# Optimization experiments

Hardware: AMD Instinct MI355X
Metric: run time of the kernel (lower is better)

## Reference

```python
import jax, jax.numpy as jnp
import numpy as np

H, P, HID, CHUNK = 8, 128, 1024, 256  # num_heads, head_dim, hidden_size, chunk_size
EPS = 1e-5


def segsum(x):
    """x: [..., L] -> [..., L, L] with out[t, s] = sum_{s+1..t} x, -inf above diagonal."""
    L = x.shape[-1]
    cs = jnp.cumsum(x, axis=-1)
    s = cs[..., :, None] - cs[..., None, :]
    mask = jnp.tril(jnp.ones((L, L), dtype=bool))
    return jnp.where(mask, s, -jnp.inf)


def ssd(X, dA, Bm, Cm, chunk):
    """Chunked Mamba2 scan (ssd_minimal_discrete).
    X:  [b, t, h, p]  (already discretized: dt * x)
    dA: [b, t, h]     (dt * A, per-head scalar decays)
    Bm, Cm: [b, t, h, n]
    """
    b, t, h, p = X.shape
    c = t // chunk
    X = X.reshape(b, c, chunk, h, p)
    Bm = Bm.reshape(b, c, chunk, h, -1)
    Cm = Cm.reshape(b, c, chunk, h, -1)
    dA = dA.reshape(b, c, chunk, h).transpose(0, 3, 1, 2)  # [b, h, c, l]
    Acs = jnp.cumsum(dA, axis=-1)                          # [b, h, c, l]
    Lm = jnp.exp(segsum(dA))                               # [b, h, c, l, l]
    # intra-chunk (diagonal blocks)
    Y_diag = jnp.einsum('bclhn,bcshn,bhcls,bcshp->bclhp', Cm, Bm, Lm, X)
    # per-chunk state contribution
    decay_states = jnp.exp(Acs[..., -1:] - Acs)            # [b, h, c, l]
    states = jnp.einsum('bclhn,bhcl,bclhp->bchpn', Bm, decay_states, X)
    # inter-chunk recurrence (vectorized via segsum over chunk decays)
    A_last = Acs[..., -1]                                  # [b, h, c]
    decay_chunk = jnp.exp(segsum(jnp.pad(A_last, ((0, 0), (0, 0), (1, 0)))))  # [b,h,c+1,c+1]
    states = jnp.concatenate([jnp.zeros_like(states[:, :1]), states], axis=1)  # [b, c+1, h, p, n]
    new_states = jnp.einsum('bhzc,bchpn->bzhpn', decay_chunk, states)
    prev = new_states[:, :-1]                              # states entering each chunk
    out_decay = jnp.exp(Acs)                               # [b, h, c, l]
    Y_off = jnp.einsum('bclhn,bchpn,bhcl->bclhp', Cm, prev, out_decay)
    return (Y_diag + Y_off).reshape(b, t, h, p)


def setup_inputs() -> dict:
    key = jax.random.key(0)
    ks = jax.random.split(key, 6)
    B, T = 2, 4096
    hidden_states = jax.random.normal(ks[0], (B, T, HID), dtype=jnp.float32)
    dt_W = 0.01 * jax.random.normal(ks[1], (H, HID), dtype=jnp.float32)
    dt_b = jnp.zeros((H,), jnp.float32)
    g_W = 0.02 * jax.random.normal(ks[2], (H, HID), dtype=jnp.float32)
    g_b = jnp.zeros((H,), jnp.float32)
    A_log = jnp.log(jnp.arange(1, H + 1, dtype=jnp.float32))
    D = jnp.ones((H,), jnp.float32)
    dt_bias = jnp.ones((H,), jnp.float32)
    norm_weight = jnp.ones((H * P,), jnp.float32)
    o_W = jax.random.normal(ks[3], (H, P, P), dtype=jnp.float32) / np.sqrt(P)
    o_b = jnp.zeros((H, P), jnp.float32)
    return dict(hidden_states=hidden_states, dt_W=dt_W, dt_b=dt_b, g_W=g_W, g_b=g_b,
                A_log=A_log, D=D, dt_bias=dt_bias, norm_weight=norm_weight, o_W=o_W, o_b=o_b)


def reference(hidden_states, dt_W, dt_b, g_W, g_b, A_log, D, dt_bias, norm_weight, o_W, o_b):
    B, T, _ = hidden_states.shape
    dt = hidden_states @ dt_W.T + dt_b                 # [B, T, H]
    gate = jnp.tanh(hidden_states @ g_W.T + g_b)       # [B, T, H]
    gate_full = jnp.repeat(gate, P, axis=-1)           # repeat_interleave -> [B, T, H*P]
    A = -jnp.exp(A_log)                                # [H]
    x = hidden_states.reshape(B, T, H, P)
    dt_eff = dt + dt_bias                              # dt_bias applied inside the kernel
    Y = ssd(x * dt_eff[..., None], dt_eff * A, x, x, CHUNK)  # B = C = x per source
    Y = Y + D[None, None, :, None] * x                 # skip term
    # RMSNormGated, norm_before_gate=False: norm(y * silu(gate))
    z = Y.reshape(B, T, H * P) * jax.nn.silu(gate_full)
    z = z * jax.lax.rsqrt(jnp.mean(z * z, axis=-1, keepdims=True) + EPS) * norm_weight
    last = z.reshape(B, T, H, P)[:, -1]                # out[:, -1, :, :]
    o = jnp.einsum('bhp,hpq->bhq', last, o_W) + o_b    # GroupLinear (per-head)
    return o.reshape(B, H * P)
```

## Files before the change

### kernel.cpp

```cpp
#include <hip/hip_runtime.h>
#include <math.h>

#define NH 8
#define NP 128
#define HID 1024
#define TT 4096
#define BB 2
#define WIN 256
#define NDT (BB * WIN / 4)

#define WS_XD 4096
#define WS_SG 8192
#define WS_ZQ 8208
#define WS_U  8224
#define WS_CTRL 10272

__global__ __launch_bounds__(256) void k_pre(const float* __restrict__ hid,
                                             const float* __restrict__ dtW,
                                             const float* __restrict__ dtb,
                                             const float* __restrict__ dtbias,
                                             const float* __restrict__ gW,
                                             const float* __restrict__ gb,
                                             float* __restrict__ dtEff,
                                             float* __restrict__ xdot,
                                             float* __restrict__ sgate_g,
                                             int* __restrict__ ctrl) {
    __shared__ float sW[NH * HID];
    __shared__ float sXL[HID];
    int tid = threadIdx.x;
    int idx = blockIdx.x;
    if (idx == 0 && tid == 0) ctrl[0] = 0;
    bool isGate = (idx >= NDT);
    int b = isGate ? (idx - NDT) : (idx >> 6);

    const float* Wsrc = isGate ? gW : dtW;
    for (int i = tid * 4; i < NH * HID; i += 1024)
        *(float4*)&sW[i] = *(const float4*)&Wsrc[i];
    const float* xl = hid + ((size_t)b * TT + TT - 1) * HID;
    *(float4*)&sXL[tid * 4] = *(const float4*)&xl[tid * 4];
    __syncthreads();

    int wave = tid >> 6, lane = tid & 63;
    int twin = isGate ? (WIN - 1) : ((idx & 63) * 4 + wave);
    const float* hrow = hid + ((size_t)b * TT + (TT - WIN) + twin) * HID;

    float acc[NH];
#pragma unroll
    for (int h = 0; h < NH; ++h) acc[h] = 0.f;
    float pd[4];

#pragma unroll
    for (int i = 0; i < 4; ++i) {
        float4 v = *(const float4*)&hrow[i * 256 + lane * 4];
#pragma unroll
        for (int h = 0; h < NH; ++h) {
            float4 w = *(const float4*)&sW[h * HID + i * 256 + lane * 4];
            acc[h] += v.x * w.x + v.y * w.y + v.z * w.z + v.w * w.w;
        }
        float4 x4 = *(const float4*)&sXL[i * 256 + lane * 4];
        pd[i] = v.x * x4.x + v.y * x4.y + v.z * x4.z + v.w * x4.w;
    }

#pragma unroll
    for (int h = 0; h < NH; ++h) {
        float a = acc[h];
#pragma unroll
        for (int off = 32; off >= 1; off >>= 1) a += __shfl_xor(a, off, 64);
        acc[h] = a;
    }

    if (isGate) {
        if (tid == 0) {
#pragma unroll
            for (int h = 0; h < NH; ++h) {
                float g = tanhf(acc[h] + gb[h]);
                sgate_g[b * NH + h] = g / (1.f + expf(-g));
            }
        }
        return;
    }

#pragma unroll
    for (int i = 0; i < 4; ++i) {
#pragma unroll
        for (int off = 16; off >= 1; off >>= 1) pd[i] += __shfl_xor(pd[i], off, 32);
    }

    if (lane == 0) {
#pragma unroll
        for (int h = 0; h < NH; ++h)
            dtEff[(b * NH + h) * WIN + twin] = acc[h] + dtb[h] + dtbias[h];
#pragma unroll
        for (int i = 0; i < 4; ++i)
            xdot[(b * NH + 2 * i) * WIN + twin] = pd[i];
    }
    if (lane == 32) {
#pragma unroll
        for (int i = 0; i < 4; ++i)
            xdot[(b * NH + 2 * i + 1) * WIN + twin] = pd[i];
    }
}

__global__ __launch_bounds__(256) void k_fin(const float* __restrict__ hid,
                                             const float* __restrict__ dtEff,
                                             const float* __restrict__ xdot,
                                             const float* __restrict__ A_log,
                                             const float* __restrict__ Dv,
                                             const float* __restrict__ sgate_g,
                                             const float* __restrict__ normw,
                                             const float* __restrict__ oW,
                                             const float* __restrict__ ob,
                                             float* __restrict__ u_g,
                                             float* __restrict__ zsq_g,
                                             int* __restrict__ ctrl,
                                             float* __restrict__ out) {
    int bh = blockIdx.x;
    int b = bh >> 3, h = bh & 7;
    int tid = threadIdx.x, wave = tid >> 6, lane = tid & 63;

    __shared__ float sWT[4];
    __shared__ float scoef[WIN];
    __shared__ int sMinR;
    __shared__ float sacc[2][NP];
    __shared__ float sred[2];
    __shared__ float szn[NP];
    __shared__ float4 sa4[8][32];
    __shared__ int sLast;

    if (tid == 0) sMinR = WIN - 1;

    float A = -expf(A_log[h]);
    float mydt = dtEff[bh * WIN + tid];
    float myxd = xdot[bh * WIN + tid];
    float dA = mydt * A;

    float x = dA;
#pragma unroll
    for (int off = 1; off < 64; off <<= 1) {
        float v = __shfl_down(x, off, 64);
        if (lane + off < 64) x += v;
    }
    if (lane == 0) sWT[wave] = x;
    __syncthreads();
    float offs = 0.f;
    for (int w = wave + 1; w < 4; ++w) offs += sWT[w];
    float e = x + offs - dA;

    float coef = 0.f;
    if (e > -104.f) {
        coef = expf(e) * mydt * myxd;
        atomicMin(&sMinR, tid);
    }
    scoef[tid] = coef;
    __syncthreads();

    int r0 = sMinR;
    int tt = tid >> 7, pp = tid & 127;
    const float* xb = hid + ((size_t)b * TT + (TT - WIN)) * HID + h * NP;
    float acc = 0.f;
    for (int r = r0 + tt; r < WIN; r += 2)
        acc += scoef[r] * xb[(size_t)r * HID + pp];
    sacc[tt][pp] = acc;
    __syncthreads();

    if (tid < NP) {
        float xlv = hid[((size_t)b * TT + TT - 1) * HID + h * NP + tid];
        float z = (sacc[0][tid] + sacc[1][tid] + Dv[h] * xlv) * sgate_g[bh];
        szn[tid] = z * normw[h * NP + tid];
        float s = z * z;
#pragma unroll
        for (int off = 32; off >= 1; off >>= 1) s += __shfl_xor(s, off, 64);
        if ((tid & 63) == 0) sred[tid >> 6] = s;
    }
    __syncthreads();
    if (tid == 0) zsq_g[bh] = sred[0] + sred[1];

    int qg = tid & 31, seg = tid >> 5;
    const float* Wb = oW + (size_t)h * NP * NP;
    float4 a = {0.f, 0.f, 0.f, 0.f};
#pragma unroll
    for (int j = 0; j < 16; ++j) {
        int p = seg * 16 + j;
        float zv = szn[p];
        float4 w = *(const float4*)&Wb[p * NP + 4 * qg];
        a.x += zv * w.x; a.y += zv * w.y; a.z += zv * w.z; a.w += zv * w.w;
    }
    sa4[seg][qg] = a;
    __syncthreads();

    if (tid < 32) {
        float4 r = sa4[0][tid];
#pragma unroll
        for (int s = 1; s < 8; ++s) {
            float4 v = sa4[s][tid];
            r.x += v.x; r.y += v.y; r.z += v.z; r.w += v.w;
        }
        *(float4*)&u_g[bh * NP + 4 * tid] = r;
    }

    __syncthreads();
    if (tid == 0) {
        __threadfence();
        int t = __hip_atomic_fetch_add(&ctrl[0], 1, __ATOMIC_ACQ_REL,
                                       __HIP_MEMORY_SCOPE_AGENT);
        sLast = (t == BB * NH - 1) ? 1 : 0;
    }
    __syncthreads();
    if (!sLast) return;
    if (tid == 0) __threadfence();
    __syncthreads();

    float s0 = 0.f, s1 = 0.f;
#pragma unroll
    for (int i = 0; i < NH; ++i) {
        s0 += zsq_g[i];
        s1 += zsq_g[NH + i];
    }
    float sc0 = rsqrtf(s0 / (float)HID + 1e-5f);
    float sc1 = rsqrtf(s1 / (float)HID + 1e-5f);

#pragma unroll
    for (int k = 0; k < 8; ++k) {
        int c = tid + k * 256;
        float sc = (c >> 10) ? sc1 : sc0;
        out[c] = u_g[c] * sc + ob[c & 1023];
    }
}

extern "C" void kernel_launch(void* const* d_in, const int* in_sizes, int n_in,
                              void* d_out, int out_size, void* d_ws, size_t ws_size,
                              hipStream_t stream) {
    const float* hid    = (const float*)d_in[0];
    const float* dtW    = (const float*)d_in[1];
    const float* dtb    = (const float*)d_in[2];
    const float* gW     = (const float*)d_in[3];
    const float* gb     = (const float*)d_in[4];
    const float* A_log  = (const float*)d_in[5];
    const float* Dv     = (const float*)d_in[6];
    const float* dtbias = (const float*)d_in[7];
    const float* normw  = (const float*)d_in[8];
    const float* oW     = (const float*)d_in[9];
    const float* ob     = (const float*)d_in[10];
    float* out = (float*)d_out;

    float* ws = (float*)d_ws;
    float* dtEff = ws;
    float* xdot  = ws + WS_XD;
    float* sgate = ws + WS_SG;
    float* zsq   = ws + WS_ZQ;
    float* u_g   = ws + WS_U;
    int*   ctrl  = (int*)(ws + WS_CTRL);

    hipLaunchKernelGGL(k_pre, dim3(NDT + BB), dim3(256), 0, stream,
                       hid, dtW, dtb, dtbias, gW, gb, dtEff, xdot, sgate, ctrl);
    hipLaunchKernelGGL(k_fin, dim3(BB * NH), dim3(256), 0, stream,
                       hid, dtEff, xdot, A_log, Dv, sgate, normw, oW, ob,
                       u_g, zsq, ctrl, out);
}
```

Baseline: 21.14 us.

## Fuse pre and final kernels into one launch with a grid-wide spin barrier

Merges the projection kernel and the scan/finalize kernel into a single 128-block kernel. Blocks write dtEff and xdot, bump an atomic counter, and the first 16 blocks spin until all blocks arrive before running the per-(b,h) scan, norm and output projection. The gate projection is moved into those 16 blocks, and the last-token row is read from shared memory instead of global. This removes one kernel launch and the gap between launches, but adds a memset node and relies on all 128 blocks being co-resident for the spin barrier.

```diff
diff --git a/kernel.cpp b/kernel.cpp
--- a/kernel.cpp
+++ b/kernel.cpp
@@ -7,42 +7,52 @@
 #define TT 4096
 #define BB 2
 #define WIN 256
-#define NDT (BB * WIN / 4)
+#define NBLK 128
+#define NWORK (BB * NH)
 
 #define WS_XD 4096
-#define WS_SG 8192
-#define WS_ZQ 8208
-#define WS_U  8224
-#define WS_CTRL 10272
-
-__global__ __launch_bounds__(256) void k_pre(const float* __restrict__ hid,
-                                             const float* __restrict__ dtW,
-                                             const float* __restrict__ dtb,
-                                             const float* __restrict__ dtbias,
-                                             const float* __restrict__ gW,
-                                             const float* __restrict__ gb,
-                                             float* __restrict__ dtEff,
-                                             float* __restrict__ xdot,
-                                             float* __restrict__ sgate_g,
-                                             int* __restrict__ ctrl) {
+#define WS_U  8192
+#define WS_ZQ 10240
+#define WS_CTRL 10256
+
+__global__ __launch_bounds__(256) void k_all(
+    const float* __restrict__ hid, const float* __restrict__ dtW,
+    const float* __restrict__ dtb, const float* __restrict__ dtbias,
+    const float* __restrict__ gW, const float* __restrict__ gb,
+    const float* __restrict__ A_log, const float* __restrict__ Dv,
+    const float* __restrict__ normw, const float* __restrict__ oW,
+    const float* __restrict__ ob, float* __restrict__ ws,
+    int* __restrict__ ctrl, float* __restrict__ out)
+{
     __shared__ float sW[NH * HID];
     __shared__ float sXL[HID];
-    int tid = threadIdx.x;
-    int idx = blockIdx.x;
-    if (idx == 0 && tid == 0) ctrl[0] = 0;
-    bool isGate = (idx >= NDT);
-    int b = isGate ? (idx - NDT) : (idx >> 6);
-
-    const float* Wsrc = isGate ? gW : dtW;
+    __shared__ float sWT[4];
+    __shared__ float sgp[4];
+    __shared__ float scoef[WIN];
+    __shared__ int   sMinR;
+    __shared__ float sacc[2][NP];
+    __shared__ float sred[2];
+    __shared__ float szn[NP];
+    __shared__ float4 sa4[8][32];
+    __shared__ int   sLast;
+
+    float* dtEff = ws;
+    float* xdot  = ws + WS_XD;
+    float* u_g   = ws + WS_U;
+    float* zsq_g = ws + WS_ZQ;
+
+    int tid = threadIdx.x, idx = blockIdx.x;
+    int wave = tid >> 6, lane = tid & 63;
+    int b1 = idx & 1;
+    int twin = (idx >> 1) * 4 + wave;
+
     for (int i = tid * 4; i < NH * HID; i += 1024)
-        *(float4*)&sW[i] = *(const float4*)&Wsrc[i];
-    const float* xl = hid + ((size_t)b * TT + TT - 1) * HID;
+        *(float4*)&sW[i] = *(const float4*)&dtW[i];
+    const float* xl = hid + ((size_t)b1 * TT + TT - 1) * HID;
     *(float4*)&sXL[tid * 4] = *(const float4*)&xl[tid * 4];
     __syncthreads();
 
-    int wave = tid >> 6, lane = tid & 63;
-    int twin = isGate ? (WIN - 1) : ((idx & 63) * 4 + wave);
-    const float* hrow = hid + ((size_t)b * TT + (TT - WIN) + twin) * HID;
+    const float* hrow = hid + ((size_t)b1 * TT + (TT - WIN) + twin) * HID;
 
     float acc[NH];
 #pragma unroll
@@ -60,7 +70,6 @@
         float4 x4 = *(const float4*)&sXL[i * 256 + lane * 4];
         pd[i] = v.x * x4.x + v.y * x4.y + v.z * x4.z + v.w * x4.w;
     }
-
 #pragma unroll
     for (int h = 0; h < NH; ++h) {
         float a = acc[h];
@@ -68,72 +77,57 @@
         for (int off = 32; off >= 1; off >>= 1) a += __shfl_xor(a, off, 64);
         acc[h] = a;
     }
-
-    if (isGate) {
-        if (tid == 0) {
-#pragma unroll
-            for (int h = 0; h < NH; ++h) {
-                float g = tanhf(acc[h] + gb[h]);
-                sgate_g[b * NH + h] = g / (1.f + expf(-g));
-            }
-        }
-        return;
-    }
-
 #pragma unroll
     for (int i = 0; i < 4; ++i) {
 #pragma unroll
         for (int off = 16; off >= 1; off >>= 1) pd[i] += __shfl_xor(pd[i], off, 32);
     }
-
     if (lane == 0) {
 #pragma unroll
         for (int h = 0; h < NH; ++h)
-            dtEff[(b * NH + h) * WIN + twin] = acc[h] + dtb[h] + dtbias[h];
+            dtEff[(b1 * NH + h) * WIN + twin] = acc[h] + dtb[h] + dtbias[h];
 #pragma unroll
         for (int i = 0; i < 4; ++i)
-            xdot[(b * NH + 2 * i) * WIN + twin] = pd[i];
+            xdot[(b1 * NH + 2 * i) * WIN + twin] = pd[i];
     }
     if (lane == 32) {
 #pragma unroll
         for (int i = 0; i < 4; ++i)
-            xdot[(b * NH + 2 * i + 1) * WIN + twin] = pd[i];
-    }
-}
-
-__global__ __launch_bounds__(256) void k_fin(const float* __restrict__ hid,
-                                             const float* __restrict__ dtEff,
-                                             const float* __restrict__ xdot,
-                                             const float* __restrict__ A_log,
-                                             const float* __restrict__ Dv,
-                                             const float* __restrict__ sgate_g,
-                                             const float* __restrict__ normw,
-                                             const float* __restrict__ oW,
-                                             const float* __restrict__ ob,
-                                             float* __restrict__ u_g,
-                                             float* __restrict__ zsq_g,
-                                             int* __restrict__ ctrl,
-                                             float* __restrict__ out) {
-    int bh = blockIdx.x;
-    int b = bh >> 3, h = bh & 7;
-    int tid = threadIdx.x, wave = tid >> 6, lane = tid & 63;
-
-    __shared__ float sWT[4];
-    __shared__ float scoef[WIN];
-    __shared__ int sMinR;
-    __shared__ float sacc[2][NP];
-    __shared__ float sred[2];
-    __shared__ float szn[NP];
-    __shared__ float4 sa4[8][32];
-    __shared__ int sLast;
-
-    if (tid == 0) sMinR = WIN - 1;
+            xdot[(b1 * NH + 2 * i + 1) * WIN + twin] = pd[i];
+    }
+
+    __syncthreads();
+    if (tid == 0) {
+        __threadfence();
+        __hip_atomic_fetch_add(&ctrl[0], 1, __ATOMIC_RELAXED,
+                               __HIP_MEMORY_SCOPE_AGENT);
+    }
+    if (idx >= NWORK) return;
+
+    if (tid == 0) {
+        while (__hip_atomic_fetch_add(&ctrl[0], 0, __ATOMIC_RELAXED,
+                                      __HIP_MEMORY_SCOPE_AGENT) < NBLK)
+            __builtin_amdgcn_s_sleep(4);
+        __threadfence();
+        sMinR = WIN - 1;
+    }
+    __syncthreads();
+
+    int b = idx & 1, h = idx >> 1;
+    int bh = b * NH + h;
 
     float A = -expf(A_log[h]);
     float mydt = dtEff[bh * WIN + tid];
     float myxd = xdot[bh * WIN + tid];
     float dA = mydt * A;
 
+    float4 g4 = *(const float4*)&gW[h * HID + tid * 4];
+    float4 xg = *(const float4*)&sXL[tid * 4];
+    float gp = g4.x * xg.x + g4.y * xg.y + g4.z * xg.z + g4.w * xg.w;
+#pragma unroll
+    for (int off = 32; off >= 1; off >>= 1) gp += __shfl_xor(gp, off, 64);
+    if (lane == 0) sgp[wave] = gp;
+
     float x = dA;
 #pragma unroll
     for (int off = 1; off < 64; off <<= 1) {
@@ -142,6 +136,7 @@
     }
     if (lane == 0) sWT[wave] = x;
     __syncthreads();
+
     float offs = 0.f;
     for (int w = wave + 1; w < 4; ++w) offs += sWT[w];
     float e = x + offs - dA;
@@ -152,20 +147,23 @@
         atomicMin(&sMinR, tid);
     }
     scoef[tid] = coef;
+
+    float gt = tanhf(sgp[0] + sgp[1] + sgp[2] + sgp[3] + gb[h]);
+    float gate = gt / (1.f + expf(-gt));
     __syncthreads();
 
     int r0 = sMinR;
     int tt = tid >> 7, pp = tid & 127;
     const float* xb = hid + ((size_t)b * TT + (TT - WIN)) * HID + h * NP;
-    float acc = 0.f;
+    float pacc = 0.f;
     for (int r = r0 + tt; r < WIN; r += 2)
-        acc += scoef[r] * xb[(size_t)r * HID + pp];
-    sacc[tt][pp] = acc;
+        pacc += scoef[r] * xb[(size_t)r * HID + pp];
+    sacc[tt][pp] = pacc;
     __syncthreads();
 
     if (tid < NP) {
-        float xlv = hid[((size_t)b * TT + TT - 1) * HID + h * NP + tid];
-        float z = (sacc[0][tid] + sacc[1][tid] + Dv[h] * xlv) * sgate_g[bh];
+        float xlv = sXL[h * NP + tid];
+        float z = (sacc[0][tid] + sacc[1][tid] + Dv[h] * xlv) * gate;
         szn[tid] = z * normw[h * NP + tid];
         float s = z * z;
 #pragma unroll
@@ -201,9 +199,9 @@
     __syncthreads();
     if (tid == 0) {
         __threadfence();
-        int t = __hip_atomic_fetch_add(&ctrl[0], 1, __ATOMIC_ACQ_REL,
+        int t = __hip_atomic_fetch_add(&ctrl[1], 1, __ATOMIC_ACQ_REL,
                                        __HIP_MEMORY_SCOPE_AGENT);
-        sLast = (t == BB * NH - 1) ? 1 : 0;
+        sLast = (t == NWORK - 1) ? 1 : 0;
     }
     __syncthreads();
     if (!sLast) return;
@@ -244,16 +242,10 @@
     float* out = (float*)d_out;
 
     float* ws = (float*)d_ws;
-    float* dtEff = ws;
-    float* xdot  = ws + WS_XD;
-    float* sgate = ws + WS_SG;
-    float* zsq   = ws + WS_ZQ;
-    float* u_g   = ws + WS_U;
-    int*   ctrl  = (int*)(ws + WS_CTRL);
-
-    hipLaunchKernelGGL(k_pre, dim3(NDT + BB), dim3(256), 0, stream,
-                       hid, dtW, dtb, dtbias, gW, gb, dtEff, xdot, sgate, ctrl);
-    hipLaunchKernelGGL(k_fin, dim3(BB * NH), dim3(256), 0, stream,
-                       hid, dtEff, xdot, A_log, Dv, sgate, normw, oW, ob,
-                       u_g, zsq, ctrl, out);
+    int* ctrl = (int*)(ws + WS_CTRL);
+
+    hipMemsetAsync(ctrl, 0, 64, stream);
+    hipLaunchKernelGGL(k_all, dim3(NBLK), dim3(256), 0, stream,
+                       hid, dtW, dtb, dtbias, gW, gb, A_log, Dv,
+                       normw, oW, ob, ws, ctrl, out);
 }
```

New measurement: 29.52 us. 1.4x slower.

## Read weights directly from global in k_pre and prefetch o_W into registers in k_fin

Applied to the files above, without the earlier changes.

k_pre stops staging the 32 KB dt/gate weight matrix and the last hidden row in shared memory. Each block now reads them straight from global memory, relying on L2/L1 cache, which removes the bulk copy and a barrier per block. k_fin issues its per-head o_W loads, plus the gate, D, last-x and norm-weight values, at kernel start so their latency overlaps the scan and reduction. The cost is 64 extra VGPRs for the o_W registers and redundant global weight reads across waves in k_pre.

```diff
diff --git a/kernel.cpp b/kernel.cpp
--- a/kernel.cpp
+++ b/kernel.cpp
@@ -25,24 +25,16 @@
                                              float* __restrict__ xdot,
                                              float* __restrict__ sgate_g,
                                              int* __restrict__ ctrl) {
-    __shared__ float sW[NH * HID];
-    __shared__ float sXL[HID];
-    int tid = threadIdx.x;
-    int idx = blockIdx.x;
+    int tid = threadIdx.x, idx = blockIdx.x;
     if (idx == 0 && tid == 0) ctrl[0] = 0;
     bool isGate = (idx >= NDT);
     int b = isGate ? (idx - NDT) : (idx >> 6);
 
-    const float* Wsrc = isGate ? gW : dtW;
-    for (int i = tid * 4; i < NH * HID; i += 1024)
-        *(float4*)&sW[i] = *(const float4*)&Wsrc[i];
-    const float* xl = hid + ((size_t)b * TT + TT - 1) * HID;
-    *(float4*)&sXL[tid * 4] = *(const float4*)&xl[tid * 4];
-    __syncthreads();
-
     int wave = tid >> 6, lane = tid & 63;
     int twin = isGate ? (WIN - 1) : ((idx & 63) * 4 + wave);
+    const float* W = isGate ? gW : dtW;
     const float* hrow = hid + ((size_t)b * TT + (TT - WIN) + twin) * HID;
+    const float* xl   = hid + ((size_t)b * TT + (TT - 1)) * HID;
 
     float acc[NH];
 #pragma unroll
@@ -54,10 +46,10 @@
         float4 v = *(const float4*)&hrow[i * 256 + lane * 4];
 #pragma unroll
         for (int h = 0; h < NH; ++h) {
-            float4 w = *(const float4*)&sW[h * HID + i * 256 + lane * 4];
+            float4 w = *(const float4*)&W[h * HID + i * 256 + lane * 4];
             acc[h] += v.x * w.x + v.y * w.y + v.z * w.z + v.w * w.w;
         }
-        float4 x4 = *(const float4*)&sXL[i * 256 + lane * 4];
+        float4 x4 = *(const float4*)&xl[i * 256 + lane * 4];
         pd[i] = v.x * x4.x + v.y * x4.y + v.z * x4.z + v.w * x4.w;
     }
 
@@ -129,6 +121,20 @@
 
     if (tid == 0) sMinR = WIN - 1;
 
+    int qg = tid & 31, seg = tid >> 5;
+    const float* Wb = oW + (size_t)h * NP * NP;
+    float4 wreg[16];
+#pragma unroll
+    for (int j = 0; j < 16; ++j)
+        wreg[j] = *(const float4*)&Wb[(seg * 16 + j) * NP + 4 * qg];
+    float gatev = sgate_g[bh];
+    float Dh = Dv[h];
+    float xlv = 0.f, nwv = 0.f;
+    if (tid < NP) {
+        xlv = hid[((size_t)b * TT + TT - 1) * HID + h * NP + tid];
+        nwv = normw[h * NP + tid];
+    }
+
     float A = -expf(A_log[h]);
     float mydt = dtEff[bh * WIN + tid];
     float myxd = xdot[bh * WIN + tid];
@@ -157,16 +163,15 @@
     int r0 = sMinR;
     int tt = tid >> 7, pp = tid & 127;
     const float* xb = hid + ((size_t)b * TT + (TT - WIN)) * HID + h * NP;
-    float acc = 0.f;
+    float pacc = 0.f;
     for (int r = r0 + tt; r < WIN; r += 2)
-        acc += scoef[r] * xb[(size_t)r * HID + pp];
-    sacc[tt][pp] = acc;
+        pacc += scoef[r] * xb[(size_t)r * HID + pp];
+    sacc[tt][pp] = pacc;
     __syncthreads();
 
     if (tid < NP) {
-        float xlv = hid[((size_t)b * TT + TT - 1) * HID + h * NP + tid];
-        float z = (sacc[0][tid] + sacc[1][tid] + Dv[h] * xlv) * sgate_g[bh];
-        szn[tid] = z * normw[h * NP + tid];
+        float z = (sacc[0][tid] + sacc[1][tid] + Dh * xlv) * gatev;
+        szn[tid] = z * nwv;
         float s = z * z;
 #pragma unroll
         for (int off = 32; off >= 1; off >>= 1) s += __shfl_xor(s, off, 64);
@@ -175,14 +180,11 @@
     __syncthreads();
     if (tid == 0) zsq_g[bh] = sred[0] + sred[1];
 
-    int qg = tid & 31, seg = tid >> 5;
-    const float* Wb = oW + (size_t)h * NP * NP;
     float4 a = {0.f, 0.f, 0.f, 0.f};
 #pragma unroll
     for (int j = 0; j < 16; ++j) {
-        int p = seg * 16 + j;
-        float zv = szn[p];
-        float4 w = *(const float4*)&Wb[p * NP + 4 * qg];
+        float zv = szn[seg * 16 + j];
+        float4 w = wreg[j];
         a.x += zv * w.x; a.y += zv * w.y; a.z += zv * w.z; a.w += zv * w.w;
     }
     sa4[seg][qg] = a;
```

Result: no change. 20.91 us (-1.1%).
